# Performance work log

Hardware: AMD Instinct MI355X
Metric: run time of the kernel (lower is better)

The kernel has to match this reference:

```python
import jax, jax.numpy as jnp
import numpy as np

B, N, D, OUT = 4, 512, 128, 128

def setup_inputs() -> dict:
    key = jax.random.key(0)
    k1, k2, k3, k4 = jax.random.split(key, 4)
    x = jax.random.normal(k1, (B, N, D), dtype=jnp.float32)
    # binary adjacency mask (float, as it multiplies edge features in the original)
    adj = (jax.random.uniform(k2, (B, N, N)) < 0.5).astype(jnp.float32)
    # nn.Linear(2D, OUT): store as (2D, OUT) so y = feat @ W + b
    W = jax.random.normal(k3, (2 * D, OUT), dtype=jnp.float32) * (1.0 / np.sqrt(2 * D))
    b = jax.random.normal(k4, (OUT,), dtype=jnp.float32) * 0.01
    return {"x": x, "adj": adj, "W": W, "b": b}

def reference(x, adj, W, b):
    # edge_feat = cat([x_i, x_j - x_i]); linear on concat decomposes as
    # x_i @ W1 + (x_j - x_i) @ W2 = x_i @ (W1 - W2) + x_j @ W2  -> avoids the (B,N,N,2D) concat.
    d = x.shape[-1]
    W1, W2 = W[:d], W[d:]
    p = jnp.einsum('bnd,do->bno', x, W1 - W2)   # contribution of x_i
    q = jnp.einsum('bnd,do->bno', x, W2)        # contribution of x_j
    pre = p[:, :, None, :] + q[:, None, :, :] + b  # (B, N, N, OUT)
    h = jax.nn.relu(pre) * adj[..., None]          # dropout is identity in eval mode
    return jnp.max(h, axis=2)                      # max over neighbors j -> (B, N, OUT)
```

## Files before the change

### kernel.cpp

```cpp
#include <hip/hip_runtime.h>

#define B_ 4
#define N_ 512
#define D_ 128
#define O_ 128

#define R1 8

__global__ __launch_bounds__(128)
void gemm_pq_kernel(const float* __restrict__ x, const float* __restrict__ W,
                    const float* __restrict__ bias, float* __restrict__ q,
                    float* __restrict__ phat) {
    const int o = threadIdx.x;
    const int row0 = blockIdx.x * R1;

    float accp[R1], accq[R1];
    const float bv = bias[o];
#pragma unroll
    for (int r = 0; r < R1; ++r) { accp[r] = bv; accq[r] = 0.0f; }

    const float* __restrict__ xb = x + (size_t)row0 * D_;

#pragma unroll 4
    for (int k = 0; k < D_; ++k) {
        const float w1 = W[(size_t)k * O_ + o];
        const float w2 = W[(size_t)(k + D_) * O_ + o];
        const float wd = w1 - w2;
#pragma unroll
        for (int r = 0; r < R1; ++r) {
            const float xv = xb[(size_t)r * D_ + k];
            accp[r] = fmaf(xv, wd, accp[r]);
            accq[r] = fmaf(xv, w2, accq[r]);
        }
    }

#pragma unroll
    for (int r = 0; r < R1; ++r) {
        const size_t idx = (size_t)(row0 + r) * O_ + o;
        q[idx]    = accq[r];
        phat[idx] = accp[r];
    }
}

#define TI 8

__global__ __launch_bounds__(512)
void maskmax_kernel(const float* __restrict__ q, const float* __restrict__ phat,
                    const float* __restrict__ adj, float* __restrict__ out) {
    const int tid = threadIdx.x;
    const int o   = tid & (O_ - 1);
    const int jq  = __builtin_amdgcn_readfirstlane(tid >> 7);
    const int b   = blockIdx.x >> 6;
    const int i0  = (blockIdx.x & 63) * TI;

    const float* __restrict__ qb   = q + (size_t)b * N_ * O_ + o;
    const float* __restrict__ arow = adj + ((size_t)b * N_ + i0) * N_;

    float m[TI];
#pragma unroll
    for (int i = 0; i < TI; ++i) m[i] = -1e30f;

    const int j0 = jq * (N_ / 4);
    for (int j = j0; j < j0 + (N_ / 4); j += 4) {
        const float qv0 = qb[(size_t)(j + 0) * O_];
        const float qv1 = qb[(size_t)(j + 1) * O_];
        const float qv2 = qb[(size_t)(j + 2) * O_];
        const float qv3 = qb[(size_t)(j + 3) * O_];
#pragma unroll
        for (int i = 0; i < TI; ++i) {
            const float* __restrict__ ar = arow + (size_t)i * N_ + j;
            const float c0 = fmaf(ar[0], 1024.0f, qv0);
            const float c1 = fmaf(ar[1], 1024.0f, qv1);
            const float c2 = fmaf(ar[2], 1024.0f, qv2);
            const float c3 = fmaf(ar[3], 1024.0f, qv3);
            m[i] = fmaxf(fmaxf(m[i], c0), c1);
            m[i] = fmaxf(fmaxf(m[i], c2), c3);
        }
    }

    __shared__ float part[4][TI][O_];
#pragma unroll
    for (int i = 0; i < TI; ++i) part[jq][i][o] = m[i];
    __syncthreads();

    for (int t = tid; t < TI * O_; t += 512) {
        const int i  = t >> 7;
        const int oo = t & (O_ - 1);
        const float mm = fmaxf(fmaxf(part[0][i][oo], part[1][i][oo]),
                               fmaxf(part[2][i][oo], part[3][i][oo]));
        const size_t idx = ((size_t)b * N_ + i0 + i) * O_ + oo;
        const float v = phat[idx] + mm - 1024.0f;
        out[idx] = v > 0.0f ? v : 0.0f;
    }
}

extern "C" void kernel_launch(void* const* d_in, const int* in_sizes, int n_in,
                              void* d_out, int out_size, void* d_ws, size_t ws_size,
                              hipStream_t stream) {
    const float* x    = (const float*)d_in[0];
    const float* adj  = (const float*)d_in[1];
    const float* W    = (const float*)d_in[2];
    const float* bias = (const float*)d_in[3];
    float* out = (float*)d_out;

    float* q    = (float*)d_ws;
    float* phat = q + (size_t)B_ * N_ * O_;

    gemm_pq_kernel<<<(B_ * N_) / R1, 128, 0, stream>>>(x, W, bias, q, phat);
    maskmax_kernel<<<B_ * (N_ / TI), 512, 0, stream>>>(q, phat, adj, out);
}
```

Measured before the change: 90.67 us.

## Split K in projection GEMM and widen neighbor split in mask-max kernel

The projection GEMM now uses 512 threads per block, with four groups each covering a quarter of the K dimension. Partial sums are combined through a padded shared-memory reduction before q and phat are written, and bias is added only after that reduction. The mask-max kernel doubles its thread count to 1024 so the neighbor dimension is split eight ways instead of four, unrolls eight j per step, and uses a padded transposed shared buffer for the final max. The aim is more parallelism on a small grid to hide latency, at the cost of extra shared-memory traffic and barriers.

```diff
diff --git a/kernel.cpp b/kernel.cpp
--- a/kernel.cpp
+++ b/kernel.cpp
@@ -7,22 +7,24 @@
 
 #define R1 8
 
-__global__ __launch_bounds__(128)
+__global__ __launch_bounds__(512)
 void gemm_pq_kernel(const float* __restrict__ x, const float* __restrict__ W,
                     const float* __restrict__ bias, float* __restrict__ q,
                     float* __restrict__ phat) {
-    const int o = threadIdx.x;
+    const int tid = threadIdx.x;
+    const int o   = tid & (O_ - 1);
+    const int kq  = __builtin_amdgcn_readfirstlane(tid >> 7);
     const int row0 = blockIdx.x * R1;
-
-    float accp[R1], accq[R1];
-    const float bv = bias[o];
-#pragma unroll
-    for (int r = 0; r < R1; ++r) { accp[r] = bv; accq[r] = 0.0f; }
 
     const float* __restrict__ xb = x + (size_t)row0 * D_;
 
+    float accp[R1], accq[R1];
+#pragma unroll
+    for (int r = 0; r < R1; ++r) { accp[r] = 0.0f; accq[r] = 0.0f; }
+
+    const int k0 = kq * (D_ / 4);
 #pragma unroll 4
-    for (int k = 0; k < D_; ++k) {
+    for (int k = k0; k < k0 + D_ / 4; ++k) {
         const float w1 = W[(size_t)k * O_ + o];
         const float w2 = W[(size_t)(k + D_) * O_ + o];
         const float wd = w1 - w2;
@@ -34,17 +36,37 @@
         }
     }
 
+    __shared__ float red[R1][O_][5];
+
 #pragma unroll
-    for (int r = 0; r < R1; ++r) {
-        const size_t idx = (size_t)(row0 + r) * O_ + o;
-        q[idx]    = accq[r];
-        phat[idx] = accp[r];
+    for (int r = 0; r < R1; ++r) red[r][o][kq] = accq[r];
+    __syncthreads();
+    {
+        for (int t = tid; t < R1 * O_; t += 512) {
+            const int r = t >> 7, oo = t & (O_ - 1);
+            const float s = (red[r][oo][0] + red[r][oo][1]) +
+                            (red[r][oo][2] + red[r][oo][3]);
+            q[(size_t)(row0 + r) * O_ + oo] = s;
+        }
+    }
+    __syncthreads();
+#pragma unroll
+    for (int r = 0; r < R1; ++r) red[r][o][kq] = accp[r];
+    __syncthreads();
+    {
+        for (int t = tid; t < R1 * O_; t += 512) {
+            const int r = t >> 7, oo = t & (O_ - 1);
+            const float s = (red[r][oo][0] + red[r][oo][1]) +
+                            (red[r][oo][2] + red[r][oo][3]);
+            phat[(size_t)(row0 + r) * O_ + oo] = s + bias[oo];
+        }
     }
 }
 
 #define TI 8
+#define JS 8
 
-__global__ __launch_bounds__(512)
+__global__ __launch_bounds__(1024)
 void maskmax_kernel(const float* __restrict__ q, const float* __restrict__ phat,
                     const float* __restrict__ adj, float* __restrict__ out) {
     const int tid = threadIdx.x;
@@ -60,34 +82,43 @@
 #pragma unroll
     for (int i = 0; i < TI; ++i) m[i] = -1e30f;
 
-    const int j0 = jq * (N_ / 4);
-    for (int j = j0; j < j0 + (N_ / 4); j += 4) {
-        const float qv0 = qb[(size_t)(j + 0) * O_];
-        const float qv1 = qb[(size_t)(j + 1) * O_];
-        const float qv2 = qb[(size_t)(j + 2) * O_];
-        const float qv3 = qb[(size_t)(j + 3) * O_];
+    const int j0 = jq * (N_ / JS);
+    for (int j = j0; j < j0 + (N_ / JS); j += 8) {
+        float qv[8];
+#pragma unroll
+        for (int u = 0; u < 8; ++u)
+            qv[u] = qb[(size_t)(j + u) * O_];
 #pragma unroll
         for (int i = 0; i < TI; ++i) {
             const float* __restrict__ ar = arow + (size_t)i * N_ + j;
-            const float c0 = fmaf(ar[0], 1024.0f, qv0);
-            const float c1 = fmaf(ar[1], 1024.0f, qv1);
-            const float c2 = fmaf(ar[2], 1024.0f, qv2);
-            const float c3 = fmaf(ar[3], 1024.0f, qv3);
-            m[i] = fmaxf(fmaxf(m[i], c0), c1);
-            m[i] = fmaxf(fmaxf(m[i], c2), c3);
+            const float c0 = fmaf(ar[0], 1024.0f, qv[0]);
+            const float c1 = fmaf(ar[1], 1024.0f, qv[1]);
+            const float c2 = fmaf(ar[2], 1024.0f, qv[2]);
+            const float c3 = fmaf(ar[3], 1024.0f, qv[3]);
+            const float c4 = fmaf(ar[4], 1024.0f, qv[4]);
+            const float c5 = fmaf(ar[5], 1024.0f, qv[5]);
+            const float c6 = fmaf(ar[6], 1024.0f, qv[6]);
+            const float c7 = fmaf(ar[7], 1024.0f, qv[7]);
+            float mi = m[i];
+            mi = fmaxf(mi, fmaxf(c0, c1));
+            mi = fmaxf(mi, fmaxf(c2, c3));
+            mi = fmaxf(mi, fmaxf(c4, c5));
+            mi = fmaxf(mi, fmaxf(c6, c7));
+            m[i] = mi;
         }
     }
 
-    __shared__ float part[4][TI][O_];
+    __shared__ float part[TI][O_][JS + 1];
 #pragma unroll
-    for (int i = 0; i < TI; ++i) part[jq][i][o] = m[i];
+    for (int i = 0; i < TI; ++i) part[i][o][jq] = m[i];
     __syncthreads();
 
-    for (int t = tid; t < TI * O_; t += 512) {
-        const int i  = t >> 7;
-        const int oo = t & (O_ - 1);
-        const float mm = fmaxf(fmaxf(part[0][i][oo], part[1][i][oo]),
-                               fmaxf(part[2][i][oo], part[3][i][oo]));
+    {
+        const int i  = tid >> 7;
+        const int oo = tid & (O_ - 1);
+        float mm = -1e30f;
+#pragma unroll
+        for (int p = 0; p < JS; ++p) mm = fmaxf(mm, part[i][oo][p]);
         const size_t idx = ((size_t)b * N_ + i0 + i) * O_ + oo;
         const float v = phat[idx] + mm - 1024.0f;
         out[idx] = v > 0.0f ? v : 0.0f;
@@ -106,6 +137,6 @@
     float* q    = (float*)d_ws;
     float* phat = q + (size_t)B_ * N_ * O_;
 
-    gemm_pq_kernel<<<(B_ * N_) / R1, 128, 0, stream>>>(x, W, bias, q, phat);
-    maskmax_kernel<<<B_ * (N_ / TI), 512, 0, stream>>>(q, phat, adj, out);
+    gemm_pq_kernel<<<(B_ * N_) / R1, 512, 0, stream>>>(x, W, bias, q, phat);
+    maskmax_kernel<<<B_ * (N_ / TI), 1024, 0, stream>>>(q, phat, adj, out);
 }
```

Measured after the change: 75.51 us. 1.2x faster.
